# Performance work log

Hardware: AMD Instinct MI355X
Metric: run time of the kernel (lower is better)

The kernel has to match this reference:

```python
import math
import jax, jax.numpy as jnp
import numpy as np

B, S, HID, NH = 1, 2048, 4096, 32
HD = HID // NH  # 128
INV_NORM = 1.0 / math.sqrt(HD)


def _build_alibi(n_heads, seq_len, batch):
    # Standard Bloom ALiBi slopes.
    cp2 = 2 ** math.floor(math.log2(n_heads))
    base = 2.0 ** (-(2.0 ** -(math.log2(cp2) - 3)))
    slopes = base ** np.arange(1, cp2 + 1)
    if cp2 != n_heads:
        extra_base = 2.0 ** (-(2.0 ** -(math.log2(2 * cp2) - 3)))
        n_rem = min(cp2, n_heads - cp2)
        slopes = np.concatenate([slopes, extra_base ** np.arange(1, 2 * n_rem + 1, 2)])
    arange = np.arange(seq_len, dtype=np.float32)[None, None, :]
    alibi = slopes[:, None, None].astype(np.float32) * arange  # [NH,1,S]
    alibi = np.broadcast_to(alibi[None], (batch, n_heads, 1, seq_len)).reshape(batch * n_heads, 1, seq_len)
    return jnp.asarray(alibi, jnp.float32)


def setup_inputs() -> dict:
    key = jax.random.key(0)
    ks = jax.random.split(key, 5)
    return {
        "hidden_states": jax.random.normal(ks[0], (B, S, HID), jnp.float32),
        "alibi": _build_alibi(NH, S, B),  # [B*NH, 1, S]
        "w_qkv": jax.random.normal(ks[1], (3 * HID, HID), jnp.float32) * 0.02,
        "b_qkv": jax.random.normal(ks[2], (3 * HID,), jnp.float32) * 0.02,
        "w_dense": jax.random.normal(ks[3], (HID, HID), jnp.float32) * 0.02,
        "b_dense": jax.random.normal(ks[4], (HID,), jnp.float32) * 0.02,
    }


def reference(hidden_states, alibi, w_qkv, b_qkv, w_dense, b_dense):
    b, s, _ = hidden_states.shape
    # Fused QKV projection, per-head interleaved layout [B,S,NH,3,HD]
    fused = hidden_states @ w_qkv.T + b_qkv
    fused = fused.reshape(b, s, NH, 3, HD)
    q = fused[..., 0, :].transpose(0, 2, 1, 3).reshape(b * NH, s, HD)
    k = fused[..., 1, :].transpose(0, 2, 1, 3).reshape(b * NH, s, HD)
    v = fused[..., 2, :].transpose(0, 2, 1, 3).reshape(b * NH, s, HD)
    # baddbmm(alibi, q, k^T, beta=1.0, alpha=inv_norm_factor)
    scores = alibi + INV_NORM * jnp.einsum("bqd,bkd->bqk", q, k)  # [B*NH,S,S]
    causal = jnp.tril(jnp.ones((s, s), dtype=bool))
    scores = jnp.where(causal[None], scores, jnp.finfo(scores.dtype).min)
    probs = jax.nn.softmax(scores.astype(jnp.float32), axis=-1).astype(hidden_states.dtype)
    ctx = jnp.einsum("bqk,bkd->bqd", probs, v)  # [B*NH,S,HD]
    ctx = ctx.reshape(b, NH, s, HD).transpose(0, 2, 1, 3).reshape(b, s, HID)
    return ctx @ w_dense.T + b_dense
```

## Files before the change

### kernel.cpp

```cpp
#include <hip/hip_runtime.h>
#include <math.h>


typedef __attribute__((ext_vector_type(8))) short short8;
typedef __attribute__((ext_vector_type(4))) float floatx4;
typedef __attribute__((ext_vector_type(4))) unsigned short ushort4v;

#define S_LEN 2048
#define HID_DIM 4096
#define NHEADS 32
#define HDIM 128
#define QKV_N 12288
#define QK_STRIDE 8192
#define INV_NORM 0.08838834764831845f

__device__ __forceinline__ unsigned short f2bf(float f) {
    union { float f; unsigned int i; } v; v.f = f;
    unsigned int u = v.i;
    return (unsigned short)((u + 0x7fffu + ((u >> 16) & 1u)) >> 16);
}

typedef __attribute__((address_space(1))) unsigned int guint;
typedef __attribute__((address_space(3))) unsigned int luint;
__device__ __forceinline__ void gl_lds16(const unsigned short* g, unsigned short* l) {
    __builtin_amdgcn_global_load_lds((guint*)g, (luint*)l, 16, 0, 0);
}

__device__ __forceinline__ void wvm8() { asm volatile("s_waitcnt vmcnt(8)" ::: "memory"); }
__device__ __forceinline__ void wvm6() { asm volatile("s_waitcnt vmcnt(6)" ::: "memory"); }
__device__ __forceinline__ void wvm4() { asm volatile("s_waitcnt vmcnt(4)" ::: "memory"); }
__device__ __forceinline__ void wvm3() { asm volatile("s_waitcnt vmcnt(3)" ::: "memory"); }
__device__ __forceinline__ void wvm0() { asm volatile("s_waitcnt vmcnt(0)" ::: "memory"); }

__device__ __forceinline__ void phase_bar() {
    __builtin_amdgcn_s_barrier();
    __builtin_amdgcn_sched_barrier(0);
}

__device__ __forceinline__ void bar_lgkm() {
    asm volatile("s_waitcnt lgkmcnt(0)" ::: "memory");
    __builtin_amdgcn_s_barrier();
    __builtin_amdgcn_sched_barrier(0);
}

__global__ __launch_bounds__(256) void cvt_bf16(
    const float* __restrict__ src, unsigned short* __restrict__ dst)
{
    size_t i = ((size_t)blockIdx.x * 256 + threadIdx.x) * 8;
    float4 x = *(const float4*)(src + i);
    float4 y = *(const float4*)(src + i + 4);
    union { unsigned u[4]; short8 s; } r;
    r.u[0] = (unsigned)f2bf(x.x) | ((unsigned)f2bf(x.y) << 16);
    r.u[1] = (unsigned)f2bf(x.z) | ((unsigned)f2bf(x.w) << 16);
    r.u[2] = (unsigned)f2bf(y.x) | ((unsigned)f2bf(y.y) << 16);
    r.u[3] = (unsigned)f2bf(y.z) | ((unsigned)f2bf(y.w) << 16);
    *(short8*)(dst + i) = r.s;
}

template <int MODE, int BM, int BN>
__global__ __launch_bounds__(512, 2) void gemm_pipe(
    const unsigned short* __restrict__ A,
    const unsigned short* __restrict__ B,
    const float* __restrict__ bias,
    unsigned short* __restrict__ Cq,
    float* __restrict__ Cf,
    unsigned short* __restrict__ vt,
    int M, int N, int K)
{
    constexpr int BK = 32;
    constexpr int MF = BM / 32;
    constexpr int NF = BN / 64;
    constexpr int WR = BM / 2;
    constexpr int WC = BN / 4;
    constexpr int BUFSH = (BM + BN) * BK;
    constexpr int LA = BM / 128;
    constexpr int BW2 = (BN - 128) / 16;

    __shared__ unsigned short lds[4 * BUFSH];

    const int t = threadIdx.x;
    const int w = t >> 6, lane = t & 63, quad = lane >> 4, l15 = lane & 15;
    const int wr = w >> 2, wc = w & 3;
    const bool hi = (w < BW2);

    const int gx = gridDim.x;
    const int nwg = gx * gridDim.y;
    const int wg = blockIdx.y * gx + blockIdx.x;
    const int swz = (wg & 7) * (nwg >> 3) + (wg >> 3);
    const int bx = swz % gx, by = swz / gx;
    const int mb = by * BM, nb = bx * BN;

    const int srow = w * 16 + (lane >> 2);
    const int schunk = (((lane & 3) ^ ((lane >> 3) & 3)) << 3);
    const unsigned short* pa = A + (size_t)(mb + srow) * K + schunk;
    const unsigned short* pb = B + (size_t)(nb + srow) * K + schunk;
    const int la_off = w * 512;
    const int lb_off = BM * BK + w * 512;

    const int fchunk = ((quad ^ ((l15 >> 1) & 3)) << 3);
    const int aoff = (wr * WR + l15) * BK + fchunk;
    const int boff = BM * BK + (wc * WC + l15) * BK + fchunk;

    floatx4 acc[MF][NF];
#pragma unroll
    for (int i = 0; i < MF; i++)
#pragma unroll
        for (int j = 0; j < NF; j++) acc[i][j] = (floatx4)0.0f;

    int kstage = 0;
    auto stage = [&](int bufi) {
        unsigned short* lb = &lds[bufi * BUFSH];
#pragma unroll
        for (int i = 0; i < LA; i++)
            gl_lds16(pa + kstage + (size_t)i * 128 * K, lb + la_off + i * 4096);
        gl_lds16(pb + kstage, lb + lb_off);
        if (hi) gl_lds16(pb + kstage + (size_t)128 * K, lb + lb_off + 4096);
        kstage += BK;
    };
    auto compute = [&](int bufi) {
        const unsigned short* lt = &lds[bufi * BUFSH];
        short8 af[MF], bfr[NF];
#pragma unroll
        for (int m = 0; m < MF; m++)
            af[m] = *(const short8*)&lt[aoff + m * 16 * BK];
#pragma unroll
        for (int n = 0; n < NF; n++)
            bfr[n] = *(const short8*)&lt[boff + n * 16 * BK];
        __builtin_amdgcn_s_setprio(1);
#pragma unroll
        for (int m = 0; m < MF; m++)
#pragma unroll
            for (int n = 0; n < NF; n++)
                acc[m][n] = __builtin_amdgcn_mfma_f32_16x16x32_bf16(af[m], bfr[n], acc[m][n], 0, 0, 0);
        __builtin_amdgcn_s_setprio(0);
    };
    auto wait_steady = [&] {
        if constexpr (LA == 2) { if (hi) wvm8(); else wvm6(); }
        else wvm6();
    };
    auto wait_tail = [&] {
        if constexpr (LA == 2) { if (hi) wvm4(); else wvm3(); }
        else wvm3();
    };

    const int NT = K / BK;

    stage(0); stage(1); stage(2);

    for (int kt = 0; kt < NT - 2; kt++) {
        wait_steady();
        phase_bar();
        if (kt < NT - 3) stage((kt + 3) & 3);
        compute(kt & 3);
    }
    wait_tail();
    phase_bar();
    compute((NT - 2) & 3);
    wvm0();
    phase_bar();
    compute((NT - 1) & 3);

    if (MODE == 1) {
#pragma unroll
        for (int j = 0; j < NF; j++) {
            int cb = nb + wc * WC + j * 16;
            int h = cb / 384;
            int type = (cb >> 7) % 3;
            int db = cb & 127;
            float bv = bias[cb + l15];
            if (type == 2) {
                unsigned short* vp = vt + ((size_t)h * HDIM + db + l15) * S_LEN;
#pragma unroll
                for (int m = 0; m < MF; m++) {
                    int rowbase = mb + wr * WR + m * 16 + quad * 4;
                    ushort4v pk;
#pragma unroll
                    for (int r = 0; r < 4; r++) pk[r] = f2bf(acc[m][j][r] + bv);
                    *(ushort4v*)&vp[rowbase] = pk;
                }
            } else {
                size_t colo = (size_t)h * 256 + type * 128 + db + l15;
#pragma unroll
                for (int m = 0; m < MF; m++) {
                    int rowbase = mb + wr * WR + m * 16 + quad * 4;
#pragma unroll
                    for (int r = 0; r < 4; r++)
                        Cq[(size_t)(rowbase + r) * QK_STRIDE + colo] =
                            f2bf(acc[m][j][r] + bv);
                }
            }
        }
    } else {
#pragma unroll
        for (int j = 0; j < NF; j++) {
            int col = nb + wc * WC + j * 16 + l15;
            float bv = bias[col];
#pragma unroll
            for (int m = 0; m < MF; m++) {
                int rowbase = mb + wr * WR + m * 16 + quad * 4;
#pragma unroll
                for (int r = 0; r < 4; r++)
                    Cf[(size_t)(rowbase + r) * N + col] = acc[m][j][r] + bv;
            }
        }
    }
}

__global__ __launch_bounds__(256) void attn_flash(
    const unsigned short* __restrict__ qk,
    const unsigned short* __restrict__ vt,
    const float* __restrict__ alibi,
    unsigned short* __restrict__ ctx)
{
    __shared__ unsigned short k_lds[64 * 136];
    __shared__ unsigned short vt_lds[128 * 72];
    __shared__ unsigned short p_lds[4 * 16 * 72];

    int h = blockIdx.x;
    int qt = (int)gridDim.y - 1 - (int)blockIdx.y;
    int qb = qt * 64;
    int t = threadIdx.x;
    int w = t >> 6, lane = t & 63, quad = lane >> 4, l15 = lane & 15;
    int qoff = h * 256;

    short8 qf[4];
    {
        int qrow = qb + w * 16 + l15;
        const unsigned short* qp = qk + (size_t)qrow * QK_STRIDE + qoff;
        for (int ks = 0; ks < 4; ks++)
            qf[ks] = *(const short8*)&qp[ks * 32 + quad * 8];
    }

    floatx4 o[8];
    for (int j = 0; j < 8; j++) o[j] = (floatx4)0.0f;
    float m_prev[4], l_prev[4];
    for (int r = 0; r < 4; r++) { m_prev[r] = -INFINITY; l_prev[r] = 0.0f; }

    int krow[4], kcol[4], vd[4], vch[4];
    for (int i = 0; i < 4; i++) {
        int idx = t + 256 * i;
        krow[i] = idx >> 4; kcol[i] = (idx & 15) * 8;
        vd[i]   = idx >> 3; vch[i] = (idx & 7) * 8;
    }
    short8 kreg[4], vreg[4];
    auto prefetch = [&](int tile) {
        int kb = tile * 64;
#pragma unroll
        for (int i = 0; i < 4; i++) {
            kreg[i] = *(const short8*)(qk + (size_t)(kb + krow[i]) * QK_STRIDE + qoff + 128 + kcol[i]);
            vreg[i] = *(const short8*)(vt + ((size_t)h * HDIM + vd[i]) * S_LEN + kb + vch[i]);
        }
    };

    int ntiles = qt + 1;
    prefetch(0);
    for (int tile = 0; tile < ntiles; tile++) {
        bar_lgkm();
#pragma unroll
        for (int i = 0; i < 4; i++) {
            *(short8*)&k_lds[krow[i] * 136 + kcol[i]] = kreg[i];
            *(short8*)&vt_lds[vd[i] * 72 + vch[i]]    = vreg[i];
        }
        if (tile + 1 < ntiles) prefetch(tile + 1);
        bar_lgkm();
        int kb = tile * 64;

        floatx4 s[4];
        for (int j = 0; j < 4; j++) s[j] = (floatx4)0.0f;
        for (int ks = 0; ks < 4; ks++) {
            for (int j = 0; j < 4; j++) {
                short8 bfr = *(const short8*)&k_lds[(j * 16 + l15) * 136 + ks * 32 + quad * 8];
                s[j] = __builtin_amdgcn_mfma_f32_16x16x32_bf16(qf[ks], bfr, s[j], 0, 0, 0);
            }
        }

        float sv[4][4];
        for (int j = 0; j < 4; j++) {
            int kcol2 = kb + j * 16 + l15;
            float al = alibi[h * S_LEN + kcol2];
            for (int r = 0; r < 4; r++) {
                int qrow = qb + w * 16 + quad * 4 + r;
                float x = s[j][r] * INV_NORM + al;
                sv[j][r] = (kcol2 <= qrow) ? x : -INFINITY;
            }
        }

        float p[4][4];
        for (int r = 0; r < 4; r++) {
            float mt = fmaxf(fmaxf(sv[0][r], sv[1][r]), fmaxf(sv[2][r], sv[3][r]));
            for (int off = 1; off < 16; off <<= 1)
                mt = fmaxf(mt, __shfl_xor(mt, off, 64));
            float m_new = fmaxf(m_prev[r], mt);
            float alpha = __expf(m_prev[r] - m_new);
            float rs = 0.0f;
            for (int j = 0; j < 4; j++) {
                float pv = __expf(sv[j][r] - m_new);
                p[j][r] = pv;
                rs += pv;
            }
            for (int off = 1; off < 16; off <<= 1)
                rs += __shfl_xor(rs, off, 64);
            l_prev[r] = l_prev[r] * alpha + rs;
            m_prev[r] = m_new;
            for (int j = 0; j < 8; j++) o[j][r] *= alpha;
        }

        {
            unsigned short* pb = &p_lds[w * 16 * 72];
            for (int j = 0; j < 4; j++)
                for (int r = 0; r < 4; r++)
                    pb[(quad * 4 + r) * 72 + j * 16 + l15] = f2bf(p[j][r]);
        }
        {
            const unsigned short* pb = &p_lds[w * 16 * 72];
            for (int ks = 0; ks < 2; ks++) {
                short8 ap = *(const short8*)&pb[l15 * 72 + ks * 32 + quad * 8];
                for (int j = 0; j < 8; j++) {
                    short8 bv = *(const short8*)&vt_lds[(j * 16 + l15) * 72 + ks * 32 + quad * 8];
                    o[j] = __builtin_amdgcn_mfma_f32_16x16x32_bf16(ap, bv, o[j], 0, 0, 0);
                }
            }
        }
    }

    for (int r = 0; r < 4; r++) {
        float linv = 1.0f / l_prev[r];
        int qrow = qb + w * 16 + quad * 4 + r;
        unsigned short* op = ctx + (size_t)qrow * HID_DIM + h * HDIM;
        for (int j = 0; j < 8; j++)
            op[j * 16 + l15] = f2bf(o[j][r] * linv);
    }
}

extern "C" void kernel_launch(void* const* d_in, const int* in_sizes, int n_in,
                              void* d_out, int out_size, void* d_ws, size_t ws_size,
                              hipStream_t stream) {
    const float* hidden  = (const float*)d_in[0];
    const float* alibi   = (const float*)d_in[1];
    const float* w_qkv   = (const float*)d_in[2];
    const float* b_qkv   = (const float*)d_in[3];
    const float* w_dense = (const float*)d_in[4];
    const float* b_dense = (const float*)d_in[5];
    float* out = (float*)d_out;

    unsigned short* ws    = (unsigned short*)d_ws;
    unsigned short* wq_bf = ws;
    unsigned short* fused = ws + (size_t)50331648;
    unsigned short* vt    = fused + (size_t)S_LEN * QK_STRIDE;
    unsigned short* hbf   = vt + (size_t)NHEADS * HDIM * S_LEN;
    unsigned short* ctx   = hbf;
    unsigned short* wd_bf = wq_bf;

    dim3 blk(256), blk512(512);
    cvt_bf16<<<dim3(4096),  blk, 0, stream>>>(hidden,  hbf);
    cvt_bf16<<<dim3(24576), blk, 0, stream>>>(w_qkv,   wq_bf);
    gemm_pipe<1, 256, 192><<<dim3(QKV_N / 192, S_LEN / 256), blk512, 0, stream>>>(
        hbf, wq_bf, b_qkv, fused, nullptr, vt, S_LEN, QKV_N, HID_DIM);
    attn_flash<<<dim3(NHEADS, S_LEN / 64), blk, 0, stream>>>(fused, vt, alibi, ctx);
    cvt_bf16<<<dim3(8192), blk, 0, stream>>>(w_dense, wd_bf);
    gemm_pipe<0, 128, 256><<<dim3(HID_DIM / 256, S_LEN / 128), blk512, 0, stream>>>(
        ctx, wd_bf, b_dense, nullptr, out, nullptr, S_LEN, HID_DIM, HID_DIM);
}
```

Before: 721.5 us.

## Double-buffer GEMM fragments, enlarge attention Q tile, swizzle LDS

```diff
diff --git a/kernel.cpp b/kernel.cpp
--- a/kernel.cpp
+++ b/kernel.cpp
@@ -117,28 +117,29 @@
         if (hi) gl_lds16(pb + kstage + (size_t)128 * K, lb + lb_off + 4096);
         kstage += BK;
     };
-    auto compute = [&](int bufi) {
+    auto ldfrag = [&](short8 (&af)[MF], short8 (&bf)[NF], int bufi) {
         const unsigned short* lt = &lds[bufi * BUFSH];
-        short8 af[MF], bfr[NF];
 #pragma unroll
         for (int m = 0; m < MF; m++)
             af[m] = *(const short8*)&lt[aoff + m * 16 * BK];
 #pragma unroll
         for (int n = 0; n < NF; n++)
-            bfr[n] = *(const short8*)&lt[boff + n * 16 * BK];
+            bf[n] = *(const short8*)&lt[boff + n * 16 * BK];
+    };
+    auto domfma = [&](short8 (&af)[MF], short8 (&bf)[NF]) {
         __builtin_amdgcn_s_setprio(1);
 #pragma unroll
         for (int m = 0; m < MF; m++)
 #pragma unroll
             for (int n = 0; n < NF; n++)
-                acc[m][n] = __builtin_amdgcn_mfma_f32_16x16x32_bf16(af[m], bfr[n], acc[m][n], 0, 0, 0);
+                acc[m][n] = __builtin_amdgcn_mfma_f32_16x16x32_bf16(af[m], bf[n], acc[m][n], 0, 0, 0);
         __builtin_amdgcn_s_setprio(0);
     };
-    auto wait_steady = [&] {
+    auto wait_2t = [&] {
         if constexpr (LA == 2) { if (hi) wvm8(); else wvm6(); }
         else wvm6();
     };
-    auto wait_tail = [&] {
+    auto wait_1t = [&] {
         if constexpr (LA == 2) { if (hi) wvm4(); else wvm3(); }
         else wvm3();
     };
@@ -146,19 +147,24 @@
     const int NT = K / BK;
 
     stage(0); stage(1); stage(2);
-
-    for (int kt = 0; kt < NT - 2; kt++) {
-        wait_steady();
+    wait_2t();
+    phase_bar();
+    short8 afA[MF], bfA[NF], afB[MF], bfB[NF];
+    ldfrag(afA, bfA, 0);
+
+    auto step = [&](int kt, short8 (&ca)[MF], short8 (&cb)[NF],
+                            short8 (&na)[MF], short8 (&nb2)[NF]) {
+        if (kt <= NT - 3) wait_1t();
+        else if (kt == NT - 2) wvm0();
         phase_bar();
-        if (kt < NT - 3) stage((kt + 3) & 3);
-        compute(kt & 3);
-    }
-    wait_tail();
-    phase_bar();
-    compute((NT - 2) & 3);
-    wvm0();
-    phase_bar();
-    compute((NT - 1) & 3);
+        if (kt + 3 < NT) stage((kt + 3) & 3);
+        if (kt + 1 < NT) ldfrag(na, nb2, (kt + 1) & 3);
+        domfma(ca, cb);
+    };
+    for (int kt = 0; kt < NT; kt += 2) {
+        step(kt,     afA, bfA, afB, bfB);
+        step(kt + 1, afB, bfB, afA, bfA);
+    }
 
     if (MODE == 1) {
 #pragma unroll
@@ -206,19 +212,19 @@
     }
 }
 
-__global__ __launch_bounds__(256) void attn_flash(
+__global__ __launch_bounds__(512, 2) void attn_flash(
     const unsigned short* __restrict__ qk,
     const unsigned short* __restrict__ vt,
     const float* __restrict__ alibi,
     unsigned short* __restrict__ ctx)
 {
-    __shared__ unsigned short k_lds[64 * 136];
-    __shared__ unsigned short vt_lds[128 * 72];
-    __shared__ unsigned short p_lds[4 * 16 * 72];
+    __shared__ unsigned short k_lds[64 * 128];
+    __shared__ unsigned short vt_lds[128 * 64];
+    __shared__ unsigned short p_lds[8 * 16 * 72];
 
     int h = blockIdx.x;
     int qt = (int)gridDim.y - 1 - (int)blockIdx.y;
-    int qb = qt * 64;
+    int qb = qt * 128;
     int t = threadIdx.x;
     int w = t >> 6, lane = t & 63, quad = lane >> 4, l15 = lane & 15;
     int qoff = h * 256;
@@ -227,57 +233,71 @@
     {
         int qrow = qb + w * 16 + l15;
         const unsigned short* qp = qk + (size_t)qrow * QK_STRIDE + qoff;
+#pragma unroll
         for (int ks = 0; ks < 4; ks++)
             qf[ks] = *(const short8*)&qp[ks * 32 + quad * 8];
     }
 
     floatx4 o[8];
+#pragma unroll
     for (int j = 0; j < 8; j++) o[j] = (floatx4)0.0f;
     float m_prev[4], l_prev[4];
+#pragma unroll
     for (int r = 0; r < 4; r++) { m_prev[r] = -INFINITY; l_prev[r] = 0.0f; }
 
-    int krow[4], kcol[4], vd[4], vch[4];
-    for (int i = 0; i < 4; i++) {
-        int idx = t + 256 * i;
+    int krow[2], kcol[2], kidx[2], vdd[2], vch[2], vidx[2];
+#pragma unroll
+    for (int i = 0; i < 2; i++) {
+        int idx = t + 512 * i;
         krow[i] = idx >> 4; kcol[i] = (idx & 15) * 8;
-        vd[i]   = idx >> 3; vch[i] = (idx & 7) * 8;
-    }
-    short8 kreg[4], vreg[4];
+        kidx[i] = (krow[i] * 128 + kcol[i]) ^ ((krow[i] & 7) << 3);
+        vdd[i]  = idx >> 3; vch[i] = (idx & 7) * 8;
+        vidx[i] = (vdd[i] * 64 + vch[i]) ^ ((vdd[i] & 7) << 3);
+    }
+    short8 kreg[2], vreg[2];
     auto prefetch = [&](int tile) {
         int kb = tile * 64;
 #pragma unroll
-        for (int i = 0; i < 4; i++) {
+        for (int i = 0; i < 2; i++) {
             kreg[i] = *(const short8*)(qk + (size_t)(kb + krow[i]) * QK_STRIDE + qoff + 128 + kcol[i]);
-            vreg[i] = *(const short8*)(vt + ((size_t)h * HDIM + vd[i]) * S_LEN + kb + vch[i]);
-        }
-    };
-
-    int ntiles = qt + 1;
+            vreg[i] = *(const short8*)(vt + ((size_t)h * HDIM + vdd[i]) * S_LEN + kb + vch[i]);
+        }
+    };
+
+    int ntiles = 2 * qt + 2;
     prefetch(0);
     for (int tile = 0; tile < ntiles; tile++) {
         bar_lgkm();
 #pragma unroll
-        for (int i = 0; i < 4; i++) {
-            *(short8*)&k_lds[krow[i] * 136 + kcol[i]] = kreg[i];
-            *(short8*)&vt_lds[vd[i] * 72 + vch[i]]    = vreg[i];
+        for (int i = 0; i < 2; i++) {
+            *(short8*)&k_lds[kidx[i]]  = kreg[i];
+            *(short8*)&vt_lds[vidx[i]] = vreg[i];
         }
         if (tile + 1 < ntiles) prefetch(tile + 1);
         bar_lgkm();
         int kb = tile * 64;
 
         floatx4 s[4];
+#pragma unroll
         for (int j = 0; j < 4; j++) s[j] = (floatx4)0.0f;
+        __builtin_amdgcn_s_setprio(1);
+#pragma unroll
         for (int ks = 0; ks < 4; ks++) {
+#pragma unroll
             for (int j = 0; j < 4; j++) {
-                short8 bfr = *(const short8*)&k_lds[(j * 16 + l15) * 136 + ks * 32 + quad * 8];
+                int row = j * 16 + l15;
+                short8 bfr = *(const short8*)&k_lds[(row * 128 + ks * 32 + quad * 8) ^ ((l15 & 7) << 3)];
                 s[j] = __builtin_amdgcn_mfma_f32_16x16x32_bf16(qf[ks], bfr, s[j], 0, 0, 0);
             }
         }
+        __builtin_amdgcn_s_setprio(0);
 
         float sv[4][4];
+#pragma unroll
         for (int j = 0; j < 4; j++) {
             int kcol2 = kb + j * 16 + l15;
             float al = alibi[h * S_LEN + kcol2];
+#pragma unroll
             for (int r = 0; r < 4; r++) {
                 int qrow = qb + w * 16 + quad * 4 + r;
                 float x = s[j][r] * INV_NORM + al;
@@ -286,47 +306,61 @@
         }
 
         float p[4][4];
+#pragma unroll
         for (int r = 0; r < 4; r++) {
             float mt = fmaxf(fmaxf(sv[0][r], sv[1][r]), fmaxf(sv[2][r], sv[3][r]));
+#pragma unroll
             for (int off = 1; off < 16; off <<= 1)
                 mt = fmaxf(mt, __shfl_xor(mt, off, 64));
             float m_new = fmaxf(m_prev[r], mt);
             float alpha = __expf(m_prev[r] - m_new);
             float rs = 0.0f;
+#pragma unroll
             for (int j = 0; j < 4; j++) {
                 float pv = __expf(sv[j][r] - m_new);
                 p[j][r] = pv;
                 rs += pv;
             }
+#pragma unroll
             for (int off = 1; off < 16; off <<= 1)
                 rs += __shfl_xor(rs, off, 64);
             l_prev[r] = l_prev[r] * alpha + rs;
             m_prev[r] = m_new;
+#pragma unroll
             for (int j = 0; j < 8; j++) o[j][r] *= alpha;
         }
 
         {
             unsigned short* pb = &p_lds[w * 16 * 72];
+#pragma unroll
             for (int j = 0; j < 4; j++)
+#pragma unroll
                 for (int r = 0; r < 4; r++)
                     pb[(quad * 4 + r) * 72 + j * 16 + l15] = f2bf(p[j][r]);
         }
         {
             const unsigned short* pb = &p_lds[w * 16 * 72];
+            __builtin_amdgcn_s_setprio(1);
+#pragma unroll
             for (int ks = 0; ks < 2; ks++) {
                 short8 ap = *(const short8*)&pb[l15 * 72 + ks * 32 + quad * 8];
+#pragma unroll
                 for (int j = 0; j < 8; j++) {
-                    short8 bv = *(const short8*)&vt_lds[(j * 16 + l15) * 72 + ks * 32 + quad * 8];
+                    int row = j * 16 + l15;
+                    short8 bv = *(const short8*)&vt_lds[(row * 64 + ks * 32 + quad * 8) ^ ((l15 & 7) << 3)];
                     o[j] = __builtin_amdgcn_mfma_f32_16x16x32_bf16(ap, bv, o[j], 0, 0, 0);
                 }
             }
-        }
-    }
-
+            __builtin_amdgcn_s_setprio(0);
+        }
+    }
+
+#pragma unroll
     for (int r = 0; r < 4; r++) {
         float linv = 1.0f / l_prev[r];
         int qrow = qb + w * 16 + quad * 4 + r;
         unsigned short* op = ctx + (size_t)qrow * HID_DIM + h * HDIM;
+#pragma unroll
         for (int j = 0; j < 8; j++)
             op[j * 16 + l15] = f2bf(o[j][r] * linv);
     }
@@ -356,7 +390,7 @@
     cvt_bf16<<<dim3(24576), blk, 0, stream>>>(w_qkv,   wq_bf);
     gemm_pipe<1, 256, 192><<<dim3(QKV_N / 192, S_LEN / 256), blk512, 0, stream>>>(
         hbf, wq_bf, b_qkv, fused, nullptr, vt, S_LEN, QKV_N, HID_DIM);
-    attn_flash<<<dim3(NHEADS, S_LEN / 64), blk, 0, stream>>>(fused, vt, alibi, ctx);
+    attn_flash<<<dim3(NHEADS, S_LEN / 128), blk512, 0, stream>>>(fused, vt, alibi, ctx);
     cvt_bf16<<<dim3(8192), blk, 0, stream>>>(w_dense, wd_bf);
     gemm_pipe<0, 128, 256><<<dim3(HID_DIM / 256, S_LEN / 128), blk512, 0, stream>>>(
         ctx, wd_bf, b_dense, nullptr, out, nullptr, S_LEN, HID_DIM, HID_DIM);
```

Measured after the change: 723.2 us. No clear change (+0.2%).
